# Performance work log

Measured on AMD Instinct MI355X. Metric: run time of the kernel, lower is better.

## Reference

```python
import jax, jax.numpy as jnp
import numpy as np

DSIZE = 1024
STRIDES = [8, 16, 32]
FSIZES = [(128, 128), (64, 64), (32, 32)]
LAYOUTS = [[16, 32], [64, 128], [256, 512]]
IOU_THR = 0.3
B, M = 16, 128


def _gen_anchors():
    # replicates BBoxAnchors.generate_anchors: anchors in (cx, cy, w, h)
    outs = []
    for stride, (fw, fh), layout in zip(STRIDES, FSIZES, LAYOUTS):
        lay = np.array([[0.0, 0.0, float(w), float(w)] for w in layout], dtype=np.float32)  # [k,4]
        vx = np.arange(0.5, fw, dtype=np.float32) * stride
        vy = np.arange(0.5, fh, dtype=np.float32) * stride
        gy, gx = np.meshgrid(vy, vx, indexing='ij')
        off = np.stack([gx, gy], axis=-1)  # [fh,fw,2]
        a = np.broadcast_to(lay, (fh, fw, len(layout), 4)).copy()
        a[..., :2] += off[:, :, None, :]
        outs.append(a.reshape(-1, 4))
    return np.concatenate(outs, axis=0)  # [A,4]


def cbox2bbox(c):
    return jnp.concatenate([c[..., :2] - c[..., 2:] * 0.5, c[..., :2] + c[..., 2:] * 0.5], axis=-1)


def box_iou_pairwise(a, b):
    # a: [A,4] xyxy, b: [M,4] xyxy -> [A,M]
    lt = jnp.maximum(a[:, None, :2], b[None, :, :2])
    rb = jnp.minimum(a[:, None, 2:], b[None, :, 2:])
    wh = jnp.clip(rb - lt, 0.0)
    inter = wh[..., 0] * wh[..., 1]
    area_a = (a[:, 2] - a[:, 0]) * (a[:, 3] - a[:, 1])
    area_b = (b[:, 2] - b[:, 0]) * (b[:, 3] - b[:, 1])
    return inter / (area_a[:, None] + area_b[None, :] - inter)


def _match(banchors, labels, bboxes):
    iou = box_iou_pairwise(banchors, bboxes)  # [A,M]
    max_iou_of_anchor = iou.max(axis=1)
    box_indice = iou.argmax(axis=1)
    max_iou_of_bbox = iou.max(axis=0)
    anchor_indice = iou.argmax(axis=0)

    def body(carry, xs):
        mioa, bi = carry
        j, a, v = xs
        return (mioa.at[a].set(v), bi.at[a].set(j)), None

    (max_iou_of_anchor, box_indice), _ = jax.lax.scan(
        body, (max_iou_of_anchor, box_indice),
        (jnp.arange(M, dtype=box_indice.dtype), anchor_indice, max_iou_of_bbox))

    denom = jnp.maximum(max_iou_of_bbox, IOU_THR)[box_indice]
    max_iou_of_anchor = jnp.where(max_iou_of_anchor < IOU_THR * 0.5, 0.0, max_iou_of_anchor)
    scores = max_iou_of_anchor / denom
    scores = jnp.where(labels[box_indice] <= 0, 0.0, scores)
    return scores, box_indice


def setup_inputs() -> dict:
    key = jax.random.key(0)
    k1, k2, k3 = jax.random.split(key, 3)
    labels = jax.random.randint(k1, (B, M), 0, 5, dtype=jnp.int32)
    cxy = jax.random.uniform(k2, (B, M, 2), dtype=jnp.float32) * DSIZE
    wh = jax.random.uniform(k3, (B, M, 2), dtype=jnp.float32) * 248.0 + 8.0
    bboxes = jnp.concatenate([cxy - wh * 0.5, cxy + wh * 0.5], axis=-1)  # xyxy
    anchors = jnp.asarray(_gen_anchors())  # [43008,4] cxcywh
    return {"labels": labels, "bboxes": bboxes, "anchors": anchors}


def reference(labels, bboxes, anchors):
    banchors = cbox2bbox(anchors)  # [A,4]
    scores, bi = jax.vmap(lambda l, b: _match(banchors, l, b))(labels, bboxes)  # [B,A],[B,A]
    matched = jnp.take_along_axis(bboxes, bi[..., None], axis=1)  # [B,A,4]
    return scores, matched
```

## Files before the change

kernel.cpp:

```cpp
#include <hip/hip_runtime.h>
#include <stdint.h>

typedef unsigned long long u64;

#define A_TOTAL 43008
#define NB 16
#define NM 128
#define SPLIT 168
#define WPB 4

__device__ __forceinline__ float exact_div(float x, float y) {
    float r;
    asm("v_rcp_f32 %0, %1" : "=v"(r) : "v"(y));
    float e  = __builtin_fmaf(-y, r, 1.0f);
    r        = __builtin_fmaf(e, r, r);
    e        = __builtin_fmaf(-y, r, 1.0f);
    r        = __builtin_fmaf(e, r, r);
    float q  = x * r;
    float rs = __builtin_fmaf(-y, q, x);
    return __builtin_fmaf(rs, r, q);
}

__device__ __forceinline__ u64 dpp_u64(u64 v, const int ctrl) {
    int lo = (int)(unsigned)v, hi = (int)(unsigned)(v >> 32);
    int plo, phi;
    switch (ctrl) {
        case 0xB1:
            plo = __builtin_amdgcn_update_dpp(lo, lo, 0xB1, 0xF, 0xF, false);
            phi = __builtin_amdgcn_update_dpp(hi, hi, 0xB1, 0xF, 0xF, false);
            break;
        case 0x4E:
            plo = __builtin_amdgcn_update_dpp(lo, lo, 0x4E, 0xF, 0xF, false);
            phi = __builtin_amdgcn_update_dpp(hi, hi, 0x4E, 0xF, 0xF, false);
            break;
        default:
            plo = __builtin_amdgcn_update_dpp(lo, lo, 0x141, 0xF, 0xF, false);
            phi = __builtin_amdgcn_update_dpp(hi, hi, 0x141, 0xF, 0xF, false);
            break;
    }
    return ((u64)(unsigned)phi << 32) | (unsigned)plo;
}

__global__ __launch_bounds__(256) void prep_kernel(
    const float4* __restrict__ bboxes, float* __restrict__ areaBp,
    u64* __restrict__ colfinal) {
#pragma clang fp contract(off)
    const int i = blockIdx.x * 256 + threadIdx.x;
    float4 v = bboxes[i];
    areaBp[i] = (v.z - v.x) * (v.w - v.y);
    colfinal[i] = 0ull;
}

__global__ __launch_bounds__(256) void fused_kernel(
    const float4* __restrict__ anchors, const float* __restrict__ bb,
    const float* __restrict__ areaBp,
    u64* __restrict__ rowkey,
    u64* __restrict__ colfinal) {
#pragma clang fp contract(off)
    const int b = blockIdx.y, tid = threadIdx.x;
    const int lane = tid & 63, wv = tid >> 6;
    const int abase = blockIdx.x * 256 + wv * 64;

    __shared__ float s_col[WPB][8][65];
    __shared__ u64   s_ck[WPB][NM];

    float4 an = anchors[abase + lane];
    float hw = an.z * 0.5f, hh = an.w * 0.5f;
    float ax1 = an.x - hw, ay1 = an.y - hh;
    float ax2 = an.x + hw, ay2 = an.y + hh;
    float areaA = (ax2 - ax1) * (ay2 - ay1);

    const float* box  = bb + (size_t)b * NM * 4;
    const float* area = areaBp + (size_t)b * NM;

    float best_v = -1.0f; int best_m = 0;
    const int bi = lane >> 3, part = lane & 7;
    const int rbase = part * 8;

    for (int c = 0; c < 16; ++c) {
#pragma unroll
        for (int i = 0; i < 8; ++i) {
            const int m = c * 8 + i;
            const float bx1 = box[4 * m + 0], by1 = box[4 * m + 1];
            const float bx2 = box[4 * m + 2], by2 = box[4 * m + 3];
            const float areaB = area[m];

            float ltx = fmaxf(ax1, bx1), lty = fmaxf(ay1, by1);
            float rbx = fminf(ax2, bx2), rby = fminf(ay2, by2);
            float wx = fmaxf(rbx - ltx, 0.0f), wy = fmaxf(rby - lty, 0.0f);
            float inter = wx * wy;
            float iou = exact_div(inter, (areaA + areaB) - inter);

            if (iou > best_v) { best_v = iou; best_m = m; }
            s_col[wv][i][lane] = iou;
        }
        float v = -1.0f; int tb = 0;
#pragma unroll
        for (int t = 0; t < 8; ++t) {
            float o = s_col[wv][bi][rbase + t];
            if (o > v) { v = o; tb = t; }
        }
        unsigned aidx = (unsigned)(abase + rbase + tb);
        u64 key = ((u64)__float_as_uint(v) << 32) | (u64)(unsigned)(~aidx);
        { u64 o = dpp_u64(key, 0xB1);  if (o > key) key = o; }
        { u64 o = dpp_u64(key, 0x4E);  if (o > key) key = o; }
        { u64 o = dpp_u64(key, 0x141); if (o > key) key = o; }
        if (part == 0) s_ck[wv][c * 8 + bi] = key;
    }

    rowkey[(size_t)b * A_TOTAL + abase + lane] =
        ((u64)__float_as_uint(best_v) << 32) | (u64)(unsigned)best_m;

    __syncthreads();
    if (tid < NM) {
        u64 k = s_ck[0][tid];
        for (int w = 1; w < WPB; ++w) if (s_ck[w][tid] > k) k = s_ck[w][tid];
        atomicMax(&colfinal[b * NM + tid], k);
    }
}

__global__ __launch_bounds__(256) void epilogue_kernel(
    const float4* __restrict__ bboxes, const int* __restrict__ labels,
    const u64* __restrict__ colfinal, const u64* __restrict__ rowkey,
    float* __restrict__ out_scores, float4* __restrict__ out_matched) {
#pragma clang fp contract(off)
    const int b = blockIdx.y, tid = threadIdx.x;
    const int a0 = blockIdx.x * 256, a = a0 + tid;

    __shared__ float4 sbox[NM];
    __shared__ float  s_cm[NM];
    __shared__ int    s_lab[NM];
    __shared__ int    ovr[256];
    ovr[tid] = -1;

    int my_ca = -1;
    if (tid < NM) {
        u64 k = colfinal[b * NM + tid];
        s_cm[tid] = __uint_as_float((unsigned)(k >> 32));
        my_ca = ~((int)(unsigned)(k & 0xFFFFFFFFull));
        sbox[tid]  = bboxes[b * NM + tid];
        s_lab[tid] = labels[b * NM + tid];
    }
    __syncthreads();
    if (tid < NM && my_ca >= a0 && my_ca < a0 + 256)
        atomicMax(&ovr[my_ca - a0], tid);
    __syncthreads();

    u64 rk = rowkey[(size_t)b * A_TOTAL + a];
    float best = __uint_as_float((unsigned)(rk >> 32));
    int   bi   = (int)(rk & 0xFFFFFFFFull);

    int o = ovr[tid];
    if (o >= 0) { bi = o; best = s_cm[o]; }

    float denom = fmaxf(s_cm[bi], 0.3f);
    float val   = (best < 0.15f) ? 0.0f : best;
    float score = val / denom;
    if (s_lab[bi] <= 0) score = 0.0f;

    out_scores[(size_t)b * A_TOTAL + a]  = score;
    out_matched[(size_t)b * A_TOTAL + a] = sbox[bi];
}

extern "C" void kernel_launch(void* const* d_in, const int* in_sizes, int n_in,
                              void* d_out, int out_size, void* d_ws, size_t ws_size,
                              hipStream_t stream) {
    const int*    labels  = (const int*)d_in[0];
    const float4* bboxes  = (const float4*)d_in[1];
    const float4* anchors = (const float4*)d_in[2];

    float* out = (float*)d_out;

    char* ws = (char*)d_ws;
    u64*   rowkey   = (u64*)ws;                      ws += (size_t)NB * A_TOTAL * 8;
    u64*   colfinal = (u64*)ws;                      ws += (size_t)NB * NM * 8;
    float* areaBp   = (float*)ws;

    prep_kernel<<<(NB * NM) / 256, 256, 0, stream>>>(bboxes, areaBp, colfinal);

    dim3 g(SPLIT, NB);
    fused_kernel<<<g, 256, 0, stream>>>(anchors, (const float*)bboxes, areaBp,
                                        rowkey, colfinal);
    epilogue_kernel<<<g, 256, 0, stream>>>(
        bboxes, labels, colfinal, rowkey,
        out, (float4*)(out + (size_t)NB * A_TOTAL));
}
```

Measured before the change: 130.0 us.

## Skip non-overlapping box chunks via per-chunk bounding boxes and wave ballots

Adds a prep step that computes a bounding rectangle for each group of 8 ground-truth boxes, then in the fused kernel skips whole chunks (and individual boxes) whose rectangles overlap no anchor in the wavefront, using wave-wide ballots. Skipped IoUs are treated as zero, so best_v starts at 0 and the column keys default to zero. This removes most of the IoU divisions and shared-memory column reductions, since anchors are small and local, at the cost of extra branching and subtle tie semantics when all IoUs are zero (argmax index choices for anchors or boxes with no overlap).

```diff
diff --git a/kernel.cpp b/kernel.cpp
--- a/kernel.cpp
+++ b/kernel.cpp
@@ -43,17 +43,30 @@
 
 __global__ __launch_bounds__(256) void prep_kernel(
     const float4* __restrict__ bboxes, float* __restrict__ areaBp,
-    u64* __restrict__ colfinal) {
+    u64* __restrict__ colfinal, float4* __restrict__ chunkbnd) {
 #pragma clang fp contract(off)
     const int i = blockIdx.x * 256 + threadIdx.x;
     float4 v = bboxes[i];
     areaBp[i] = (v.z - v.x) * (v.w - v.y);
     colfinal[i] = 0ull;
+    if (blockIdx.x == 0) {
+        const int t = threadIdx.x;
+        const int base = (t >> 4) * NM + (t & 15) * 8;
+        float4 f = bboxes[base];
+        float mnx = f.x, mny = f.y, mxx = f.z, mxy = f.w;
+#pragma unroll
+        for (int k = 1; k < 8; ++k) {
+            float4 u = bboxes[base + k];
+            mnx = fminf(mnx, u.x); mny = fminf(mny, u.y);
+            mxx = fmaxf(mxx, u.z); mxy = fmaxf(mxy, u.w);
+        }
+        chunkbnd[t] = make_float4(mnx, mny, mxx, mxy);
+    }
 }
 
 __global__ __launch_bounds__(256) void fused_kernel(
     const float4* __restrict__ anchors, const float* __restrict__ bb,
-    const float* __restrict__ areaBp,
+    const float* __restrict__ areaBp, const float4* __restrict__ chunkbnd,
     u64* __restrict__ rowkey,
     u64* __restrict__ colfinal) {
 #pragma clang fp contract(off)
@@ -64,6 +77,9 @@
     __shared__ float s_col[WPB][8][65];
     __shared__ u64   s_ck[WPB][NM];
 
+    s_ck[wv][lane] = 0ull;
+    s_ck[wv][64 + lane] = 0ull;
+
     float4 an = anchors[abase + lane];
     float hw = an.z * 0.5f, hh = an.w * 0.5f;
     float ax1 = an.x - hw, ay1 = an.y - hh;
@@ -72,36 +88,49 @@
 
     const float* box  = bb + (size_t)b * NM * 4;
     const float* area = areaBp + (size_t)b * NM;
-
-    float best_v = -1.0f; int best_m = 0;
+    const float4* cb  = chunkbnd + (b << 4);
+
+    float best_v = 0.0f; int best_m = 0;
     const int bi = lane >> 3, part = lane & 7;
     const int rbase = part * 8;
 
     for (int c = 0; c < 16; ++c) {
+        float4 g = cb[c];
+        bool cl = (g.z > ax1) & (g.x < ax2) & (g.w > ay1) & (g.y < ay2);
+        if (__ballot(cl) == 0ull) continue;
+
+        unsigned mask = 0;
 #pragma unroll
         for (int i = 0; i < 8; ++i) {
             const int m = c * 8 + i;
             const float bx1 = box[4 * m + 0], by1 = box[4 * m + 1];
             const float bx2 = box[4 * m + 2], by2 = box[4 * m + 3];
-            const float areaB = area[m];
-
-            float ltx = fmaxf(ax1, bx1), lty = fmaxf(ay1, by1);
-            float rbx = fminf(ax2, bx2), rby = fminf(ay2, by2);
-            float wx = fmaxf(rbx - ltx, 0.0f), wy = fmaxf(rby - lty, 0.0f);
-            float inter = wx * wy;
-            float iou = exact_div(inter, (areaA + areaB) - inter);
-
-            if (iou > best_v) { best_v = iou; best_m = m; }
-            s_col[wv][i][lane] = iou;
+            bool lv = (bx2 > ax1) & (bx1 < ax2) & (by2 > ay1) & (by1 < ay2);
+            if (__ballot(lv) != 0ull) {
+                mask |= 1u << i;
+                const float areaB = area[m];
+                float ltx = fmaxf(ax1, bx1), lty = fmaxf(ay1, by1);
+                float rbx = fminf(ax2, bx2), rby = fminf(ay2, by2);
+                float wx = fmaxf(rbx - ltx, 0.0f), wy = fmaxf(rby - lty, 0.0f);
+                float inter = wx * wy;
+                float iou = exact_div(inter, (areaA + areaB) - inter);
+                if (iou > best_v) { best_v = iou; best_m = m; }
+                s_col[wv][i][lane] = iou;
+            }
         }
-        float v = -1.0f; int tb = 0;
+        if (mask == 0u) continue;
+
+        u64 key = 0ull;
+        if (mask & (1u << bi)) {
+            float v = -1.0f; int tb = 0;
 #pragma unroll
-        for (int t = 0; t < 8; ++t) {
-            float o = s_col[wv][bi][rbase + t];
-            if (o > v) { v = o; tb = t; }
+            for (int t = 0; t < 8; ++t) {
+                float o = s_col[wv][bi][rbase + t];
+                if (o > v) { v = o; tb = t; }
+            }
+            unsigned aidx = (unsigned)(abase + rbase + tb);
+            key = ((u64)__float_as_uint(v) << 32) | (u64)(unsigned)(~aidx);
         }
-        unsigned aidx = (unsigned)(abase + rbase + tb);
-        u64 key = ((u64)__float_as_uint(v) << 32) | (u64)(unsigned)(~aidx);
         { u64 o = dpp_u64(key, 0xB1);  if (o > key) key = o; }
         { u64 o = dpp_u64(key, 0x4E);  if (o > key) key = o; }
         { u64 o = dpp_u64(key, 0x141); if (o > key) key = o; }
@@ -172,15 +201,17 @@
     float* out = (float*)d_out;
 
     char* ws = (char*)d_ws;
-    u64*   rowkey   = (u64*)ws;                      ws += (size_t)NB * A_TOTAL * 8;
-    u64*   colfinal = (u64*)ws;                      ws += (size_t)NB * NM * 8;
-    float* areaBp   = (float*)ws;
-
-    prep_kernel<<<(NB * NM) / 256, 256, 0, stream>>>(bboxes, areaBp, colfinal);
+    u64*    rowkey   = (u64*)ws;                     ws += (size_t)NB * A_TOTAL * 8;
+    u64*    colfinal = (u64*)ws;                     ws += (size_t)NB * NM * 8;
+    float*  areaBp   = (float*)ws;                   ws += (size_t)NB * NM * 4;
+    float4* chunkbnd = (float4*)ws;
+
+    prep_kernel<<<(NB * NM) / 256, 256, 0, stream>>>(bboxes, areaBp, colfinal,
+                                                     chunkbnd);
 
     dim3 g(SPLIT, NB);
     fused_kernel<<<g, 256, 0, stream>>>(anchors, (const float*)bboxes, areaBp,
-                                        rowkey, colfinal);
+                                        chunkbnd, rowkey, colfinal);
     epilogue_kernel<<<g, 256, 0, stream>>>(
         bboxes, labels, colfinal, rowkey,
         out, (float4*)(out + (size_t)NB * A_TOTAL));
```

Result: faster. 105.2 us (-19.1%).
